# Performance work log

Hardware: AMD Instinct MI355X
Metric: run time of the kernel (lower is better)

Reference implementation:

```python
import jax, jax.numpy as jnp
import numpy as np

N = 16384      # number of points
DIM = 128      # feature dim
POS_DIM = 3
K = 16         # neighbors (init kwarg k)
SCALE = np.float32(np.sqrt(DIM))


def setup_inputs() -> dict:
    key = jax.random.key(0)
    ks = jax.random.split(key, 16)
    g = lambda i, shape: (jax.random.normal(ks[i], shape, dtype=jnp.float32) * 0.05)
    return {
        "x": jax.random.normal(ks[0], (N, DIM), dtype=jnp.float32),
        "pos": jax.random.uniform(ks[1], (N, POS_DIM), dtype=jnp.float32),
        # weights stored as (in, out); torch Linear applies x @ W.T + b
        "Wq": g(2, (DIM, DIM)),
        "Wk": g(3, (DIM, DIM)),
        "Wv": g(4, (DIM, DIM)),
        "mid_w1": g(5, (DIM, DIM)), "mid_b1": g(6, (DIM,)),
        "mid_w2": g(7, (DIM, DIM)), "mid_b2": g(8, (DIM,)),
        "pe_w1": g(9, (POS_DIM, DIM)), "pe_b1": g(10, (DIM,)),
        "pe_w2": g(11, (DIM, DIM)), "pe_b2": g(12, (DIM,)),
        "fin_w": g(13, (DIM, DIM)), "fin_b": g(14, (DIM,)),
    }


def _knn_indices(pos):
    # squared pairwise distances [N, N]; top-K smallest -> neighbor indices [N, K]
    sq = jnp.sum(pos * pos, axis=-1)
    d2 = sq[:, None] + sq[None, :] - 2.0 * (pos @ pos.T)
    _, ind = jax.lax.top_k(-d2, K)
    return ind


def reference(x, pos, Wq, Wk, Wv, mid_w1, mid_b1, mid_w2, mid_b2,
              pe_w1, pe_b1, pe_w2, pe_b2, fin_w, fin_b):
    ind = _knn_indices(pos)                    # [N, K] int32 (constant wrt grads)
    x_k = x[ind]                               # [N, K, D]
    pos_k = pos[ind]                           # [N, K, 3]
    rel = pos[:, None, :] - pos_k              # [N, K, 3]
    pe = jax.nn.relu(rel @ pe_w1 + pe_b1) @ pe_w2 + pe_b2    # [N, K, D]
    q = x @ Wq                                 # [N, D]
    h = q[:, None, :] - (x_k @ Wk) + pe        # [N, K, D]
    y = jax.nn.relu(h @ mid_w1 + mid_b1) @ mid_w2 + mid_b2   # [N, K, D]
    y = jax.nn.softmax(y / SCALE, axis=-2)     # softmax over neighbors K
    z = x_k @ Wv + pe                          # [N, K, D]
    agg = jnp.sum(y * z, axis=-2)              # [N, D]
    return agg @ fin_w + fin_b + x
```

## Files before the change

kernel.cpp:

```cpp
#include <hip/hip_runtime.h>
#include <hip/hip_bf16.h>

#define N_PTS 16384
#define DIMF  128
#define KNB   16
#define GRES  8
#define NCELL (GRES*GRES*GRES)

typedef __attribute__((ext_vector_type(8))) short bf16x8;
typedef __attribute__((ext_vector_type(4))) short bf16x4;
typedef __attribute__((ext_vector_type(4))) float f32x4;
typedef __attribute__((ext_vector_type(4))) unsigned int u32x4;
typedef __attribute__((ext_vector_type(2))) unsigned int u32x2;

__device__ __forceinline__ unsigned short f2b(float f){
  unsigned int u = __float_as_uint(f);
  u = u + 0x7fffu + ((u >> 16) & 1u);
  return (unsigned short)(u >> 16);
}
__device__ __forceinline__ unsigned cvtpk(float lo, float hi){
  unsigned r;
  asm("v_cvt_pk_bf16_f32 %0, %1, %2" : "=v"(r) : "v"(lo), "v"(hi));
  return r;
}
__device__ __forceinline__ float b2f(unsigned short u){
  return __uint_as_float(((unsigned)u) << 16);
}
__device__ __forceinline__ float b2fs(short s){
  return __uint_as_float(((unsigned)(unsigned short)s) << 16);
}
__device__ __forceinline__ float unsort_f(unsigned s){
  unsigned u = (s & 0x80000000u) ? (s ^ 0x80000000u) : ~s;
  return __uint_as_float(u);
}

__global__ __launch_bounds__(256) void count_kernel(const float* __restrict__ pos, int* __restrict__ cnt){
  int i = blockIdx.x*256 + threadIdx.x;
  float px = pos[i*3+0], py = pos[i*3+1], pz = pos[i*3+2];
  int cx = min(GRES-1, max(0,(int)(px*(float)GRES)));
  int cy = min(GRES-1, max(0,(int)(py*(float)GRES)));
  int cz = min(GRES-1, max(0,(int)(pz*(float)GRES)));
  atomicAdd(&cnt[(cz*GRES+cy)*GRES+cx], 1);
}

__global__ __launch_bounds__(256) void scan_kernel(const int* __restrict__ cnt, int* __restrict__ starts, int* __restrict__ fillp){
  __shared__ int wsum[4];
  int t = threadIdx.x;
  int lane = t & 63, w = t >> 6;
  int a = cnt[2*t], b = cnt[2*t+1];
  int s = a + b;
  int p = s;
  #pragma unroll
  for (int off = 1; off < 64; off <<= 1){
    int v = __shfl_up(p, off, 64);
    if (lane >= off) p += v;
  }
  if (lane == 63) wsum[w] = p;
  __syncthreads();
  int base = 0;
  for (int i = 0; i < w; ++i) base += wsum[i];
  int excl = base + p - s;
  starts[2*t]   = excl;     fillp[2*t]   = excl;
  starts[2*t+1] = excl + a; fillp[2*t+1] = excl + a;
}

__global__ __launch_bounds__(256) void scatter_pack(const float* __restrict__ pos, int* __restrict__ fillp,
                                                    float4* __restrict__ pos4, int* __restrict__ pidx,
                                                    int* __restrict__ inv,
                                                    const float* __restrict__ w0, const float* __restrict__ w1,
                                                    const float* __restrict__ w2, const float* __restrict__ w3,
                                                    const float* __restrict__ w4, const float* __restrict__ w5,
                                                    const float* __restrict__ w6,
                                                    short* __restrict__ dst){
  if (blockIdx.x < 64){
    int i = blockIdx.x*256 + threadIdx.x;
    float px = pos[i*3+0], py = pos[i*3+1], pz = pos[i*3+2];
    int cx = min(GRES-1, max(0,(int)(px*(float)GRES)));
    int cy = min(GRES-1, max(0,(int)(py*(float)GRES)));
    int cz = min(GRES-1, max(0,(int)(pz*(float)GRES)));
    int c = (cz*GRES+cy)*GRES+cx;
    float sq = __fadd_rn(__fadd_rn(__fmul_rn(px,px), __fmul_rn(py,py)), __fmul_rn(pz,pz));
    int s = atomicAdd(&fillp[c], 1);
    pos4[s] = make_float4(px, py, pz, sq);
    pidx[s] = i;
    inv[i] = s;
  } else {
    int pb = blockIdx.x - 64;
    int slot = pb >> 6;
    const float* src = (slot==0)?w0:(slot==1)?w1:(slot==2)?w2:(slot==3)?w3:(slot==4)?w4:(slot==5)?w5:w6;
    int f = (pb & 63)*256 + threadIdx.x;
    int j  = f & 7;
    int ln = (f >> 3) & 63;
    int ks = (f >> 9) & 3;
    int nt = f >> 11;
    int k = ks*32 + ((ln >> 4) << 3) + j;
    int n = nt*16 + (ln & 15);
    dst[slot*16384 + f] = (short)f2b(src[k*DIMF + n]);
  }
}

__global__ __launch_bounds__(256) void knn_query64(const float4* __restrict__ pos4, const int* __restrict__ pidx,
                                                   const int* __restrict__ starts, const int* __restrict__ cnt,
                                                   const int* __restrict__ inv,
                                                   int* __restrict__ ind_slot, char* __restrict__ flags){
  __shared__ unsigned long long cand[4][64];
  int lane = threadIdx.x & 63;
  int wv   = threadIdx.x >> 6;
  int t = blockIdx.x*4 + wv;
  float4 qp = pos4[t];
  float qx = qp.x, qy = qp.y, qz = qp.z, qsq = qp.w;
  int cx = min(GRES-1, max(0,(int)(qx*(float)GRES)));
  int cy = min(GRES-1, max(0,(int)(qy*(float)GRES)));
  int cz = min(GRES-1, max(0,(int)(qz*(float)GRES)));
  int zlo = max(0,cz-1), zhi = min(GRES-1,cz+1);
  int ylo = max(0,cy-1), yhi = min(GRES-1,cy+1);
  int xlo = max(0,cx-1), xhi = min(GRES-1,cx+1);

  int nb = 0;
  if (lane < 27){
    int dz = lane/9 - 1, dy = (lane/3)%3 - 1, dx = lane%3 - 1;
    int zz = cz+dz, yy = cy+dy, xx = cx+dx;
    if (zz>=zlo && zz<=zhi && yy>=ylo && yy<=yhi && xx>=xlo && xx<=xhi)
      nb = cnt[(zz*GRES+yy)*GRES+xx];
  }
  #pragma unroll
  for (int o=1;o<64;o<<=1) nb += __shfl_xor(nb, o, 64);
  float V = (float)((zhi-zlo+1)*(yhi-ylo+1)*(xhi-xlo+1)) * 0.001953125f;
  float r3 = 3.8197186f * V / (float)nb;
  float tau2 = 2.0f * __powf(r3, 0.66666667f);

  int nfound = 0;
  bool okscan = false;
  for (int it = 0; it < 8; ++it){
    nfound = 0;
    for (int zz=zlo; zz<=zhi; ++zz)
    for (int yy=ylo; yy<=yhi; ++yy)
    for (int xx=xlo; xx<=xhi; ++xx){
      int c = (zz*GRES+yy)*GRES+xx;
      int s0 = starts[c], n = cnt[c];
      for (int b = 0; b < n; b += 64){
        int o = b + lane;
        bool valid = o < n;
        float d = 3.0e38f; int idx = 0;
        if (valid){
          float4 pc = pos4[s0+o];
          idx = pidx[s0+o];
          float dot = __fmaf_rn(qz, pc.z, __fmaf_rn(qy, pc.y, __fmul_rn(qx, pc.x)));
          d   = __fsub_rn(__fadd_rn(qsq, pc.w), __fmul_rn(2.0f, dot));
        }
        bool admit = valid && (d < tau2);
        unsigned long long mask = __ballot(admit);
        if (admit){
          int pos = nfound + (int)__popcll(mask & ((1ull<<lane)-1ull));
          if (pos < 64){
            unsigned su = __float_as_uint(d);
            su ^= (unsigned)((int)su >> 31) | 0x80000000u;
            cand[wv][pos] = ((unsigned long long)su << 32) | (unsigned)idx;
          }
        }
        nfound += (int)__popcll(mask);
      }
    }
    if (nfound > 64){ tau2 *= 0.7f; continue; }
    if (nfound < 16){ tau2 *= 2.0f; continue; }
    okscan = true; break;
  }
  if (!okscan){ if (lane == 0) flags[t] = 1; return; }

  asm volatile("s_waitcnt lgkmcnt(0)" ::: "memory");
  __builtin_amdgcn_sched_barrier(0);
  unsigned long long key = (lane < nfound) ? cand[wv][lane] : ~0ull;

  #pragma unroll
  for (int k = 2; k <= 64; k <<= 1){
    #pragma unroll
    for (int j = k>>1; j >= 1; j >>= 1){
      unsigned long long other = __shfl_xor(key, j, 64);
      bool takeSmall = (((lane & k) == 0) != ((lane & j) != 0));
      bool less = other < key;
      key = (takeSmall == less) ? other : key;
    }
  }
  if (lane < 16) ind_slot[t*KNB + lane] = inv[(int)(unsigned)(key & 0xffffffffu)];

  unsigned long long k15 = __shfl(key, 15, 64);
  float b16 = unsort_f((unsigned)(k15 >> 32));
  double mg = 1.0e300;
  double dqx=(double)qx, dqy=(double)qy, dqz=(double)qz;
  const double h = 0.125;
  if (cx-1 > 0)      mg = fmin(mg, dqx - (double)(cx-1)*h);
  if (cx+1 < GRES-1) mg = fmin(mg, (double)(cx+2)*h - dqx);
  if (cy-1 > 0)      mg = fmin(mg, dqy - (double)(cy-1)*h);
  if (cy+1 < GRES-1) mg = fmin(mg, (double)(cy+2)*h - dqy);
  if (cz-1 > 0)      mg = fmin(mg, dqz - (double)(cz-1)*h);
  if (cz+1 < GRES-1) mg = fmin(mg, (double)(cz+2)*h - dqz);
  bool ok = (mg*mg > (double)b16 + 1.0e-5);
  if (lane == 0) flags[t] = ok ? 0 : 1;
}

__global__ __launch_bounds__(256) void knn_fallback(const float4* __restrict__ pos4, const int* __restrict__ pidx,
                                                    const int* __restrict__ starts, const int* __restrict__ cnt,
                                                    const int* __restrict__ inv,
                                                    const char* __restrict__ flags, int* __restrict__ ind_slot){
  int t = blockIdx.x*256 + threadIdx.x;
  if (t >= N_PTS || !flags[t]) return;
  float4 qp = pos4[t];
  float qx = qp.x, qy = qp.y, qz = qp.z, qsq = qp.w;
  int cx = min(GRES-1, max(0,(int)(qx*(float)GRES)));
  int cy = min(GRES-1, max(0,(int)(qy*(float)GRES)));
  int cz = min(GRES-1, max(0,(int)(qz*(float)GRES)));
  float bd[KNB]; int bi[KNB];
  #pragma unroll
  for (int k=0;k<KNB;++k){ bd[k] = 3.0e38f; bi[k] = 0x7fffffff; }
  const double cinv = 0.125;
  for (int r = 0; r < GRES; ++r){
    int zlo = max(0, cz-r), zhi = min(GRES-1, cz+r);
    int ylo = max(0, cy-r), yhi = min(GRES-1, cy+r);
    int xlo = max(0, cx-r), xhi = min(GRES-1, cx+r);
    for (int zz = zlo; zz <= zhi; ++zz){
      for (int yy = ylo; yy <= yhi; ++yy){
        for (int xx = xlo; xx <= xhi; ++xx){
          int ring = max(abs(zz-cz), max(abs(yy-cy), abs(xx-cx)));
          if (ring != r) continue;
          int c = (zz*GRES+yy)*GRES+xx;
          int s0 = starts[c], e = s0 + cnt[c];
          for (int s = s0; s < e; ++s){
            float4 pc = pos4[s];
            int idx = pidx[s];
            float dot = __fmaf_rn(qz, pc.z, __fmaf_rn(qy, pc.y, __fmul_rn(qx, pc.x)));
            float d   = __fsub_rn(__fadd_rn(qsq, pc.w), __fmul_rn(2.0f, dot));
            bool adm = (d < bd[KNB-1]) || (d == bd[KNB-1] && idx < bi[KNB-1]);
            if (adm){
              #pragma unroll
              for (int p = KNB-1; p >= 1; --p){
                float pd = bd[p-1]; int pi = bi[p-1];
                bool sh  = (pd > d) || (pd == d && pi > idx);
                bool ins = (!sh) && ((bd[p] > d) || (bd[p] == d && bi[p] > idx));
                bd[p] = sh ? pd : (ins ? d   : bd[p]);
                bi[p] = sh ? pi : (ins ? idx : bi[p]);
              }
              bool s0b = (bd[0] > d) || (bd[0] == d && bi[0] > idx);
              if (s0b){ bd[0] = d; bi[0] = idx; }
            }
          }
        }
      }
    }
    if (bd[KNB-1] < 3.0e37f){
      double mg = 1.0e300;
      double dqx=(double)qx, dqy=(double)qy, dqz=(double)qz;
      if (cx - r > 0)      mg = fmin(mg, dqx - (double)(cx-r)*cinv);
      if (cx + r < GRES-1) mg = fmin(mg, (double)(cx+r+1)*cinv - dqx);
      if (cy - r > 0)      mg = fmin(mg, dqy - (double)(cy-r)*cinv);
      if (cy + r < GRES-1) mg = fmin(mg, (double)(cy+r+1)*cinv - dqy);
      if (cz - r > 0)      mg = fmin(mg, dqz - (double)(cz-r)*cinv);
      if (cz + r < GRES-1) mg = fmin(mg, (double)(cz+r+1)*cinv - dqz);
      if (mg*mg > (double)bd[KNB-1] + 1.0e-5) break;
    }
  }
  #pragma unroll
  for (int k=0;k<KNB;++k) ind_slot[t*KNB + k] = inv[bi[k]];
}

__global__ __launch_bounds__(256) void proj_kernel(const float* __restrict__ x, const int* __restrict__ pidx,
                                                   const short* __restrict__ pw,
                                                   unsigned short* __restrict__ q, unsigned short* __restrict__ xk,
                                                   unsigned short* __restrict__ xv){
  __shared__ __align__(16) char Abuf[16384];
  int tid = threadIdx.x, lane = tid & 63, wv = tid >> 6;
  int r0 = blockIdx.x * 64;
  {
    int row = tid >> 2, q4 = tid & 3;
    int orig = pidx[r0 + row];
    const float4* xr = (const float4*)(x + (size_t)orig*DIMF + q4*32);
    #pragma unroll
    for (int i=0;i<4;++i){
      float4 a = xr[2*i], b = xr[2*i+1];
      u32x4 u;
      u[0] = cvtpk(a.x, a.y); u[1] = cvtpk(a.z, a.w);
      u[2] = cvtpk(b.x, b.y); u[3] = cvtpk(b.z, b.w);
      *(u32x4*)(&Abuf[row*256 + ((q4*64 + i*16) ^ ((row&7)<<4))]) = u;
    }
  }
  __syncthreads();
  #pragma unroll 1
  for (int w = 0; w < 3; ++w){
    const bf16x8* bw = (const bf16x8*)(pw + w*16384);
    unsigned short* dst = (w==0) ? q : (w==1) ? xk : xv;
    f32x4 acc[8];
    #pragma unroll
    for (int nt=0;nt<8;++nt) acc[nt] = (f32x4){0.f,0.f,0.f,0.f};
    #pragma unroll
    for (int ks=0;ks<4;++ks){
      int ra = wv*16 + (lane&15);
      int cb = ks*64 + ((lane>>4)<<4);
      bf16x8 a0 = *(const bf16x8*)(&Abuf[ra*256 + (cb ^ ((ra&7)<<4))]);
      #pragma unroll
      for (int nt=0;nt<8;++nt){
        bf16x8 b = bw[(nt*4+ks)*64 + lane];
        acc[nt] = __builtin_amdgcn_mfma_f32_16x16x32_bf16(a0, b, acc[nt], 0, 0, 0);
      }
    }
    #pragma unroll
    for (int nt=0;nt<8;++nt){
      int grow = r0 + wv*16 + ((lane>>4)<<2);
      int col = nt*16 + (lane&15);
      unsigned pk01 = cvtpk(acc[nt][0], acc[nt][1]);
      unsigned pk23 = cvtpk(acc[nt][2], acc[nt][3]);
      dst[(size_t)(grow+0)*DIMF + col] = (unsigned short)pk01;
      dst[(size_t)(grow+1)*DIMF + col] = (unsigned short)(pk01 >> 16);
      dst[(size_t)(grow+2)*DIMF + col] = (unsigned short)pk23;
      dst[(size_t)(grow+3)*DIMF + col] = (unsigned short)(pk23 >> 16);
    }
  }
}

__global__ __launch_bounds__(512, 2) void main_kernel(
    const float* __restrict__ x, const float4* __restrict__ pos4, const int* __restrict__ pidx,
    const float* __restrict__ pe_w1, const float* __restrict__ pe_b1, const float* __restrict__ pe_b2,
    const float* __restrict__ mid_b1, const float* __restrict__ mid_b2, const float* __restrict__ fin_b,
    const unsigned short* __restrict__ qarr, const unsigned short* __restrict__ xkarr,
    const unsigned short* __restrict__ xvarr,
    const int* __restrict__ ind_slot, const short* __restrict__ pw,
    float* __restrict__ out)
{
  __shared__ __align__(16) char peLDS[32768];
  __shared__ __align__(16) char wbuf[32768];
  __shared__ float aggT[DIMF][9];
  __shared__ int indbuf[128];
  __shared__ int origbuf[8];
  int tid = threadIdx.x;
  int lane = tid & 63;
  int wv = tid >> 6;
  int t0 = blockIdx.x * 8;

  int g = lane >> 4, kl = lane & 15;
  int mt = wv;

  #define STAGE_W(slot) { \
    const char* gsrc = (const char*)(pw + (size_t)(slot)*16384) + wv*4096 + lane*16; \
    char* ldst = &wbuf[wv*4096]; \
    __builtin_amdgcn_global_load_lds(gsrc,        ldst,        16, 0, 0); \
    __builtin_amdgcn_global_load_lds(gsrc + 1024, ldst + 1024, 16, 0, 0); \
    __builtin_amdgcn_global_load_lds(gsrc + 2048, ldst + 2048, 16, 0, 0); \
    __builtin_amdgcn_global_load_lds(gsrc + 3072, ldst + 3072, 16, 0, 0); }

  if (tid < 128) indbuf[tid] = ind_slot[blockIdx.x*128 + tid];
  if (tid < 8) origbuf[tid] = pidx[t0 + tid];
  STAGE_W(3);
  __syncthreads();

  int nb4[4];
  #pragma unroll
  for (int r=0;r<4;++r) nb4[r] = indbuf[mt*16 + g*4 + r];
  int nbr = indbuf[mt*16 + kl];
  unsigned short zraw[8][4];
  #pragma unroll
  for (int nt=0;nt<8;++nt)
    #pragma unroll
    for (int r=0;r<4;++r)
      zraw[nt][r] = xvarr[(size_t)nb4[r]*DIMF + nt*16 + kl];

  bf16x8 tfrag[4];
  {
    float4 pq = pos4[t0+mt];
    float4 pn = pos4[nbr];
    float rx = pq.x-pn.x, ry = pq.y-pn.y, rz = pq.z-pn.z;
    #pragma unroll
    for (int ks=0;ks<4;++ks){
      int c0 = ks*32 + g*8;
      const float4* w0 = (const float4*)(pe_w1 + c0);
      const float4* w1 = (const float4*)(pe_w1 + DIMF + c0);
      const float4* w2 = (const float4*)(pe_w1 + 2*DIMF + c0);
      const float4* bb = (const float4*)(pe_b1 + c0);
      float4 wa0=w0[0], wa1=w0[1], wb0=w1[0], wb1=w1[1], wc0=w2[0], wc1=w2[1], wd0=bb[0], wd1=bb[1];
      float wa[8]={wa0.x,wa0.y,wa0.z,wa0.w,wa1.x,wa1.y,wa1.z,wa1.w};
      float wb[8]={wb0.x,wb0.y,wb0.z,wb0.w,wb1.x,wb1.y,wb1.z,wb1.w};
      float wc[8]={wc0.x,wc0.y,wc0.z,wc0.w,wc1.x,wc1.y,wc1.z,wc1.w};
      float wd[8]={wd0.x,wd0.y,wd0.z,wd0.w,wd1.x,wd1.y,wd1.z,wd1.w};
      float tv[8];
      #pragma unroll
      for (int j=0;j<8;++j)
        tv[j] = fmaxf(fmaf(rx, wa[j], fmaf(ry, wb[j], fmaf(rz, wc[j], wd[j]))), 0.f);
      u32x4 u;
      u[0] = cvtpk(tv[0], tv[1]); u[1] = cvtpk(tv[2], tv[3]);
      u[2] = cvtpk(tv[4], tv[5]); u[3] = cvtpk(tv[6], tv[7]);
      tfrag[ks] = __builtin_bit_cast(bf16x8, u);
    }
  }

  f32x4 acc[8];
  const bf16x8* bw = (const bf16x8*)wbuf;

  {
    #pragma unroll
    for (int nt=0;nt<8;++nt){
      float bv = pe_b2[nt*16 + kl];
      acc[nt] = (f32x4){bv,bv,bv,bv};
    }
    #pragma unroll
    for (int ks=0;ks<4;++ks){
      #pragma unroll
      for (int nt=0;nt<8;++nt){
        bf16x8 b = bw[(nt*4+ks)*64 + lane];
        acc[nt] = __builtin_amdgcn_mfma_f32_16x16x32_bf16(tfrag[ks], b, acc[nt], 0, 0, 0);
      }
    }
  }

  bf16x4 zb[8];
  int r0w = mt*16 + g*4;
  #pragma unroll
  for (int nt=0;nt<8;++nt){
    int col = nt*16 + kl;
    float p0 = acc[nt][0], p1 = acc[nt][1], p2 = acc[nt][2], p3 = acc[nt][3];
    unsigned pk01 = cvtpk(p0, p1), pk23 = cvtpk(p2, p3);
    *(unsigned short*)&peLDS[(r0w+0)*256 + ((col*2) ^ (((r0w+0)&7)<<4))] = (unsigned short)pk01;
    *(unsigned short*)&peLDS[(r0w+1)*256 + ((col*2) ^ (((r0w+1)&7)<<4))] = (unsigned short)(pk01 >> 16);
    *(unsigned short*)&peLDS[(r0w+2)*256 + ((col*2) ^ (((r0w+2)&7)<<4))] = (unsigned short)pk23;
    *(unsigned short*)&peLDS[(r0w+3)*256 + ((col*2) ^ (((r0w+3)&7)<<4))] = (unsigned short)(pk23 >> 16);
    float z0 = b2f(zraw[nt][0]) + p0;
    float z1 = b2f(zraw[nt][1]) + p1;
    float z2 = b2f(zraw[nt][2]) + p2;
    float z3 = b2f(zraw[nt][3]) + p3;
    u32x2 zu; zu[0] = cvtpk(z0, z1); zu[1] = cvtpk(z2, z3);
    zb[nt] = __builtin_bit_cast(bf16x4, zu);
  }

  bf16x8 q8[4], k8[4];
  {
    const unsigned short* qrow = qarr + (size_t)(t0+mt)*DIMF;
    const unsigned short* krow = xkarr + (size_t)nbr*DIMF;
    #pragma unroll
    for (int ks=0;ks<4;++ks){
      int c0 = ks*32 + g*8;
      q8[ks] = *(const bf16x8*)(qrow + c0);
      k8[ks] = *(const bf16x8*)(krow + c0);
    }
  }
  __syncthreads();
  STAGE_W(4);

  bf16x8 hfrag[4];
  {
    int row = mt*16 + kl;
    #pragma unroll
    for (int ks=0;ks<4;++ks){
      int c0 = ks*32 + g*8;
      bf16x8 p8 = *(const bf16x8*)(&peLDS[row*256 + ((c0*2) ^ ((row&7)<<4))]);
      float hf[8];
      #pragma unroll
      for (int j=0;j<8;++j)
        hf[j] = (b2fs(q8[ks][j]) - b2fs(k8[ks][j])) + b2fs(p8[j]);
      u32x4 u;
      u[0] = cvtpk(hf[0], hf[1]); u[1] = cvtpk(hf[2], hf[3]);
      u[2] = cvtpk(hf[4], hf[5]); u[3] = cvtpk(hf[6], hf[7]);
      hfrag[ks] = __builtin_bit_cast(bf16x8, u);
    }
  }
  __syncthreads();

  {
    #pragma unroll
    for (int nt=0;nt<8;++nt){
      float bv = mid_b1[nt*16 + kl];
      acc[nt] = (f32x4){bv,bv,bv,bv};
    }
    #pragma unroll
    for (int ks=0;ks<4;++ks){
      #pragma unroll
      for (int nt=0;nt<8;++nt){
        bf16x8 b = bw[(nt*4+ks)*64 + lane];
        acc[nt] = __builtin_amdgcn_mfma_f32_16x16x32_bf16(hfrag[ks], b, acc[nt], 0, 0, 0);
      }
    }
  }
  __syncthreads();
  STAGE_W(5);
  #pragma unroll
  for (int nt=0;nt<8;++nt){
    int col = nt*16 + kl;
    unsigned pk01 = cvtpk(fmaxf(acc[nt][0],0.f), fmaxf(acc[nt][1],0.f));
    unsigned pk23 = cvtpk(fmaxf(acc[nt][2],0.f), fmaxf(acc[nt][3],0.f));
    *(unsigned short*)&peLDS[(r0w+0)*256 + ((col*2) ^ (((r0w+0)&7)<<4))] = (unsigned short)pk01;
    *(unsigned short*)&peLDS[(r0w+1)*256 + ((col*2) ^ (((r0w+1)&7)<<4))] = (unsigned short)(pk01 >> 16);
    *(unsigned short*)&peLDS[(r0w+2)*256 + ((col*2) ^ (((r0w+2)&7)<<4))] = (unsigned short)pk23;
    *(unsigned short*)&peLDS[(r0w+3)*256 + ((col*2) ^ (((r0w+3)&7)<<4))] = (unsigned short)(pk23 >> 16);
  }
  __syncthreads();

  {
    #pragma unroll
    for (int nt=0;nt<8;++nt){
      float bv = mid_b2[nt*16 + kl];
      acc[nt] = (f32x4){bv,bv,bv,bv};
    }
    #pragma unroll
    for (int ks=0;ks<4;++ks){
      int ra = mt*16 + kl;
      int cb = ks*64 + g*16;
      bf16x8 a0 = *(const bf16x8*)(&peLDS[ra*256 + (cb ^ ((ra&7)<<4))]);
      #pragma unroll
      for (int nt=0;nt<8;++nt){
        bf16x8 b = bw[(nt*4+ks)*64 + lane];
        acc[nt] = __builtin_amdgcn_mfma_f32_16x16x32_bf16(a0, b, acc[nt], 0, 0, 0);
      }
    }
  }
  __syncthreads();
  STAGE_W(6);

  {
    const float invS = 0.08838834764831843f;
    #pragma unroll
    for (int nt=0;nt<8;++nt){
      f32x4 y = acc[nt];
      float mx = fmaxf(fmaxf(y[0],y[1]), fmaxf(y[2],y[3]));
      mx = fmaxf(mx, __shfl_xor(mx, 16, 64));
      mx = fmaxf(mx, __shfl_xor(mx, 32, 64));
      float e0 = __expf((y[0]-mx)*invS);
      float e1 = __expf((y[1]-mx)*invS);
      float e2 = __expf((y[2]-mx)*invS);
      float e3 = __expf((y[3]-mx)*invS);
      float ssum = e0+e1+e2+e3;
      ssum += __shfl_xor(ssum, 16, 64);
      ssum += __shfl_xor(ssum, 32, 64);
      bf16x4 zv = zb[nt];
      float ps = (e0*b2fs(zv[0]) + e1*b2fs(zv[1]) + e2*b2fs(zv[2]) + e3*b2fs(zv[3])) / ssum;
      ps += __shfl_xor(ps, 16, 64);
      ps += __shfl_xor(ps, 32, 64);
      if (lane < 16) aggT[nt*16 + lane][mt] = ps;
    }
  }
  __syncthreads();

  {
    f32x4 facc = (f32x4){0.f,0.f,0.f,0.f};
    #pragma unroll
    for (int ks=0;ks<4;++ks){
      int c0 = ks*32 + g*8;
      float av[8];
      #pragma unroll
      for (int j=0;j<8;++j)
        av[j] = (kl < 8) ? aggT[c0+j][kl] : 0.f;
      u32x4 u;
      u[0] = cvtpk(av[0], av[1]); u[1] = cvtpk(av[2], av[3]);
      u[2] = cvtpk(av[4], av[5]); u[3] = cvtpk(av[6], av[7]);
      bf16x8 a = __builtin_bit_cast(bf16x8, u);
      bf16x8 b = bw[(wv*4+ks)*64 + lane];
      facc = __builtin_amdgcn_mfma_f32_16x16x32_bf16(a, b, facc, 0, 0, 0);
    }
    int col = wv*16 + kl;
    float fb = fin_b[col];
    if (g < 2){
      #pragma unroll
      for (int r=0;r<4;++r){
        int prow = g*4 + r;
        int o = origbuf[prow];
        out[(size_t)o*DIMF + col] = facc[r] + fb + x[(size_t)o*DIMF + col];
      }
    }
  }
  #undef STAGE_W
}

extern "C" void kernel_launch(void* const* d_in, const int* in_sizes, int n_in,
                              void* d_out, int out_size, void* d_ws, size_t ws_size,
                              hipStream_t stream)
{
  (void)in_sizes; (void)n_in; (void)out_size; (void)ws_size;
  const float* x      = (const float*)d_in[0];
  const float* pos    = (const float*)d_in[1];
  const float* Wq     = (const float*)d_in[2];
  const float* Wk     = (const float*)d_in[3];
  const float* Wv     = (const float*)d_in[4];
  const float* mid_w1 = (const float*)d_in[5];
  const float* mid_b1 = (const float*)d_in[6];
  const float* mid_w2 = (const float*)d_in[7];
  const float* mid_b2 = (const float*)d_in[8];
  const float* pe_w1  = (const float*)d_in[9];
  const float* pe_b1  = (const float*)d_in[10];
  const float* pe_w2  = (const float*)d_in[11];
  const float* pe_b2  = (const float*)d_in[12];
  const float* fin_w  = (const float*)d_in[13];
  const float* fin_b  = (const float*)d_in[14];
  float* out = (float*)d_out;
  char* ws = (char*)d_ws;

  int*    cellcnt = (int*)   (ws + 0);
  int*    fillp   = (int*)   (ws + 4096);
  int*    starts  = (int*)   (ws + 8192);
  char*   flags   = (char*)  (ws + 18432);
  int*    pidx    = (int*)   (ws + 49152);
  float4* pos4    = (float4*)(ws + 114688);
  int*    ind     = (int*)   (ws + 376832);
  short*  pw      = (short*) (ws + 1425408);
  int*    inv     = (int*)   (ws + 1654784);
  unsigned short* qarr  = (unsigned short*)(ws + 1720320);
  unsigned short* xkarr = (unsigned short*)(ws + 5914624);
  unsigned short* xvarr = (unsigned short*)(ws + 10108928);

  hipMemsetAsync(cellcnt, 0, NCELL*sizeof(int), stream);
  count_kernel  <<<N_PTS/256, 256, 0, stream>>>(pos, cellcnt);
  scan_kernel   <<<1,         256, 0, stream>>>(cellcnt, starts, fillp);
  scatter_pack  <<<64 + 7*64, 256, 0, stream>>>(pos, fillp, pos4, pidx, inv,
                                                Wq, Wk, Wv, pe_w2, mid_w1, mid_w2, fin_w, pw);
  knn_query64   <<<N_PTS/4,   256, 0, stream>>>(pos4, pidx, starts, cellcnt, inv, ind, flags);
  knn_fallback  <<<N_PTS/256, 256, 0, stream>>>(pos4, pidx, starts, cellcnt, inv, flags, ind);
  proj_kernel   <<<N_PTS/64,  256, 0, stream>>>(x, pidx, pw, qarr, xkarr, xvarr);
  main_kernel   <<<N_PTS/8,   512, 0, stream>>>(x, pos4, pidx, pe_w1, pe_b1, pe_b2, mid_b1, mid_b2, fin_b,
                                                qarr, xkarr, xvarr, ind, pw, out);
}
```

Baseline: 163.0 us.

## Fuse kNN fallback into query kernel and prune cells beyond threshold

Adds a per-cell minimum-distance test so cells that cannot contain points within the current radius threshold are skipped during the 3x3x3 scan. The separate fallback kernel and flags array are removed; the fallback ring search now runs inline in the query wavefront, which removes one launch and the global flags round trip. The inline fallback runs the same serial per-query work redundantly on all 64 lanes of the wave, and a rare slow query now stalls its whole block.

```diff
diff --git a/kernel.cpp b/kernel.cpp
--- a/kernel.cpp
+++ b/kernel.cpp
@@ -102,7 +102,7 @@
 __global__ __launch_bounds__(256) void knn_query64(const float4* __restrict__ pos4, const int* __restrict__ pidx,
                                                    const int* __restrict__ starts, const int* __restrict__ cnt,
                                                    const int* __restrict__ inv,
-                                                   int* __restrict__ ind_slot, char* __restrict__ flags){
+                                                   int* __restrict__ ind_slot){
   __shared__ unsigned long long cand[4][64];
   int lane = threadIdx.x & 63;
   int wv   = threadIdx.x >> 6;
@@ -115,6 +115,8 @@
   int zlo = max(0,cz-1), zhi = min(GRES-1,cz+1);
   int ylo = max(0,cy-1), yhi = min(GRES-1,cy+1);
   int xlo = max(0,cx-1), xhi = min(GRES-1,cx+1);
+  const double h = 0.125;
+  double dqx=(double)qx, dqy=(double)qy, dqz=(double)qz;
 
   int nb = 0;
   if (lane < 27){
@@ -136,6 +138,11 @@
     for (int zz=zlo; zz<=zhi; ++zz)
     for (int yy=ylo; yy<=yhi; ++yy)
     for (int xx=xlo; xx<=xhi; ++xx){
+      double mdx = fmax(0.0, fmax((double)xx*h - dqx, dqx - (double)(xx+1)*h));
+      double mdy = fmax(0.0, fmax((double)yy*h - dqy, dqy - (double)(yy+1)*h));
+      double mdz = fmax(0.0, fmax((double)zz*h - dqz, dqz - (double)(zz+1)*h));
+      double md2 = mdx*mdx + mdy*mdy + mdz*mdz;
+      if (md2 > (double)tau2 + 1.0e-5) continue;
       int c = (zz*GRES+yy)*GRES+xx;
       int s0 = starts[c], n = cnt[c];
       for (int b = 0; b < n; b += 64){
@@ -165,101 +172,85 @@
     if (nfound < 16){ tau2 *= 2.0f; continue; }
     okscan = true; break;
   }
-  if (!okscan){ if (lane == 0) flags[t] = 1; return; }
-
-  asm volatile("s_waitcnt lgkmcnt(0)" ::: "memory");
-  __builtin_amdgcn_sched_barrier(0);
-  unsigned long long key = (lane < nfound) ? cand[wv][lane] : ~0ull;
-
-  #pragma unroll
-  for (int k = 2; k <= 64; k <<= 1){
-    #pragma unroll
-    for (int j = k>>1; j >= 1; j >>= 1){
-      unsigned long long other = __shfl_xor(key, j, 64);
-      bool takeSmall = (((lane & k) == 0) != ((lane & j) != 0));
-      bool less = other < key;
-      key = (takeSmall == less) ? other : key;
-    }
-  }
-  if (lane < 16) ind_slot[t*KNB + lane] = inv[(int)(unsigned)(key & 0xffffffffu)];
-
-  unsigned long long k15 = __shfl(key, 15, 64);
-  float b16 = unsort_f((unsigned)(k15 >> 32));
-  double mg = 1.0e300;
-  double dqx=(double)qx, dqy=(double)qy, dqz=(double)qz;
-  const double h = 0.125;
-  if (cx-1 > 0)      mg = fmin(mg, dqx - (double)(cx-1)*h);
-  if (cx+1 < GRES-1) mg = fmin(mg, (double)(cx+2)*h - dqx);
-  if (cy-1 > 0)      mg = fmin(mg, dqy - (double)(cy-1)*h);
-  if (cy+1 < GRES-1) mg = fmin(mg, (double)(cy+2)*h - dqy);
-  if (cz-1 > 0)      mg = fmin(mg, dqz - (double)(cz-1)*h);
-  if (cz+1 < GRES-1) mg = fmin(mg, (double)(cz+2)*h - dqz);
-  bool ok = (mg*mg > (double)b16 + 1.0e-5);
-  if (lane == 0) flags[t] = ok ? 0 : 1;
-}
-
-__global__ __launch_bounds__(256) void knn_fallback(const float4* __restrict__ pos4, const int* __restrict__ pidx,
-                                                    const int* __restrict__ starts, const int* __restrict__ cnt,
-                                                    const int* __restrict__ inv,
-                                                    const char* __restrict__ flags, int* __restrict__ ind_slot){
-  int t = blockIdx.x*256 + threadIdx.x;
-  if (t >= N_PTS || !flags[t]) return;
-  float4 qp = pos4[t];
-  float qx = qp.x, qy = qp.y, qz = qp.z, qsq = qp.w;
-  int cx = min(GRES-1, max(0,(int)(qx*(float)GRES)));
-  int cy = min(GRES-1, max(0,(int)(qy*(float)GRES)));
-  int cz = min(GRES-1, max(0,(int)(qz*(float)GRES)));
-  float bd[KNB]; int bi[KNB];
-  #pragma unroll
-  for (int k=0;k<KNB;++k){ bd[k] = 3.0e38f; bi[k] = 0x7fffffff; }
-  const double cinv = 0.125;
-  for (int r = 0; r < GRES; ++r){
-    int zlo = max(0, cz-r), zhi = min(GRES-1, cz+r);
-    int ylo = max(0, cy-r), yhi = min(GRES-1, cy+r);
-    int xlo = max(0, cx-r), xhi = min(GRES-1, cx+r);
-    for (int zz = zlo; zz <= zhi; ++zz){
-      for (int yy = ylo; yy <= yhi; ++yy){
-        for (int xx = xlo; xx <= xhi; ++xx){
-          int ring = max(abs(zz-cz), max(abs(yy-cy), abs(xx-cx)));
-          if (ring != r) continue;
-          int c = (zz*GRES+yy)*GRES+xx;
-          int s0 = starts[c], e = s0 + cnt[c];
-          for (int s = s0; s < e; ++s){
-            float4 pc = pos4[s];
-            int idx = pidx[s];
-            float dot = __fmaf_rn(qz, pc.z, __fmaf_rn(qy, pc.y, __fmul_rn(qx, pc.x)));
-            float d   = __fsub_rn(__fadd_rn(qsq, pc.w), __fmul_rn(2.0f, dot));
-            bool adm = (d < bd[KNB-1]) || (d == bd[KNB-1] && idx < bi[KNB-1]);
-            if (adm){
-              #pragma unroll
-              for (int p = KNB-1; p >= 1; --p){
-                float pd = bd[p-1]; int pi = bi[p-1];
-                bool sh  = (pd > d) || (pd == d && pi > idx);
-                bool ins = (!sh) && ((bd[p] > d) || (bd[p] == d && bi[p] > idx));
-                bd[p] = sh ? pd : (ins ? d   : bd[p]);
-                bi[p] = sh ? pi : (ins ? idx : bi[p]);
-              }
-              bool s0b = (bd[0] > d) || (bd[0] == d && bi[0] > idx);
-              if (s0b){ bd[0] = d; bi[0] = idx; }
+
+  bool needfb = !okscan;
+  if (okscan){
+    asm volatile("s_waitcnt lgkmcnt(0)" ::: "memory");
+    __builtin_amdgcn_sched_barrier(0);
+    unsigned long long key = (lane < nfound) ? cand[wv][lane] : ~0ull;
+
+    #pragma unroll
+    for (int k = 2; k <= 64; k <<= 1){
+      #pragma unroll
+      for (int j = k>>1; j >= 1; j >>= 1){
+        unsigned long long other = __shfl_xor(key, j, 64);
+        bool takeSmall = (((lane & k) == 0) != ((lane & j) != 0));
+        bool less = other < key;
+        key = (takeSmall == less) ? other : key;
+      }
+    }
+    if (lane < 16) ind_slot[t*KNB + lane] = inv[(int)(unsigned)(key & 0xffffffffu)];
+
+    unsigned long long k15 = __shfl(key, 15, 64);
+    float b16 = unsort_f((unsigned)(k15 >> 32));
+    double mg = 1.0e300;
+    if (cx-1 > 0)      mg = fmin(mg, dqx - (double)(cx-1)*h);
+    if (cx+1 < GRES-1) mg = fmin(mg, (double)(cx+2)*h - dqx);
+    if (cy-1 > 0)      mg = fmin(mg, dqy - (double)(cy-1)*h);
+    if (cy+1 < GRES-1) mg = fmin(mg, (double)(cy+2)*h - dqy);
+    if (cz-1 > 0)      mg = fmin(mg, dqz - (double)(cz-1)*h);
+    if (cz+1 < GRES-1) mg = fmin(mg, (double)(cz+2)*h - dqz);
+    needfb = !(mg*mg > (double)b16 + 1.0e-5);
+  }
+
+  if (needfb){
+    float bd[KNB]; int bi[KNB];
+    #pragma unroll
+    for (int k=0;k<KNB;++k){ bd[k] = 3.0e38f; bi[k] = 0x7fffffff; }
+    for (int r = 0; r < GRES; ++r){
+      int zl = max(0, cz-r), zh = min(GRES-1, cz+r);
+      int yl = max(0, cy-r), yh = min(GRES-1, cy+r);
+      int xl = max(0, cx-r), xh = min(GRES-1, cx+r);
+      for (int zz = zl; zz <= zh; ++zz)
+      for (int yy = yl; yy <= yh; ++yy)
+      for (int xx = xl; xx <= xh; ++xx){
+        int ring = max(abs(zz-cz), max(abs(yy-cy), abs(xx-cx)));
+        if (ring != r) continue;
+        int c = (zz*GRES+yy)*GRES+xx;
+        int s0 = starts[c], e = s0 + cnt[c];
+        for (int s = s0; s < e; ++s){
+          float4 pc = pos4[s];
+          int idx = pidx[s];
+          float dot = __fmaf_rn(qz, pc.z, __fmaf_rn(qy, pc.y, __fmul_rn(qx, pc.x)));
+          float d   = __fsub_rn(__fadd_rn(qsq, pc.w), __fmul_rn(2.0f, dot));
+          bool adm = (d < bd[KNB-1]) || (d == bd[KNB-1] && idx < bi[KNB-1]);
+          if (adm){
+            #pragma unroll
+            for (int p = KNB-1; p >= 1; --p){
+              float pd = bd[p-1]; int pi = bi[p-1];
+              bool sh  = (pd > d) || (pd == d && pi > idx);
+              bool ins = (!sh) && ((bd[p] > d) || (bd[p] == d && bi[p] > idx));
+              bd[p] = sh ? pd : (ins ? d   : bd[p]);
+              bi[p] = sh ? pi : (ins ? idx : bi[p]);
             }
+            bool s0b = (bd[0] > d) || (bd[0] == d && bi[0] > idx);
+            if (s0b){ bd[0] = d; bi[0] = idx; }
           }
         }
       }
-    }
-    if (bd[KNB-1] < 3.0e37f){
-      double mg = 1.0e300;
-      double dqx=(double)qx, dqy=(double)qy, dqz=(double)qz;
-      if (cx - r > 0)      mg = fmin(mg, dqx - (double)(cx-r)*cinv);
-      if (cx + r < GRES-1) mg = fmin(mg, (double)(cx+r+1)*cinv - dqx);
-      if (cy - r > 0)      mg = fmin(mg, dqy - (double)(cy-r)*cinv);
-      if (cy + r < GRES-1) mg = fmin(mg, (double)(cy+r+1)*cinv - dqy);
-      if (cz - r > 0)      mg = fmin(mg, dqz - (double)(cz-r)*cinv);
-      if (cz + r < GRES-1) mg = fmin(mg, (double)(cz+r+1)*cinv - dqz);
-      if (mg*mg > (double)bd[KNB-1] + 1.0e-5) break;
-    }
-  }
-  #pragma unroll
-  for (int k=0;k<KNB;++k) ind_slot[t*KNB + k] = inv[bi[k]];
+      if (bd[KNB-1] < 3.0e37f){
+        double mg = 1.0e300;
+        if (cx - r > 0)      mg = fmin(mg, dqx - (double)(cx-r)*h);
+        if (cx + r < GRES-1) mg = fmin(mg, (double)(cx+r+1)*h - dqx);
+        if (cy - r > 0)      mg = fmin(mg, dqy - (double)(cy-r)*h);
+        if (cy + r < GRES-1) mg = fmin(mg, (double)(cy+r+1)*h - dqy);
+        if (cz - r > 0)      mg = fmin(mg, dqz - (double)(cz-r)*h);
+        if (cz + r < GRES-1) mg = fmin(mg, (double)(cz+r+1)*h - dqz);
+        if (mg*mg > (double)bd[KNB-1] + 1.0e-5) break;
+      }
+    }
+    if (lane < 16) ind_slot[t*KNB + lane] = inv[bi[lane]];
+  }
 }
 
 __global__ __launch_bounds__(256) void proj_kernel(const float* __restrict__ x, const int* __restrict__ pidx,
@@ -590,7 +581,6 @@
   int*    cellcnt = (int*)   (ws + 0);
   int*    fillp   = (int*)   (ws + 4096);
   int*    starts  = (int*)   (ws + 8192);
-  char*   flags   = (char*)  (ws + 18432);
   int*    pidx    = (int*)   (ws + 49152);
   float4* pos4    = (float4*)(ws + 114688);
   int*    ind     = (int*)   (ws + 376832);
@@ -605,8 +595,7 @@
   scan_kernel   <<<1,         256, 0, stream>>>(cellcnt, starts, fillp);
   scatter_pack  <<<64 + 7*64, 256, 0, stream>>>(pos, fillp, pos4, pidx, inv,
                                                 Wq, Wk, Wv, pe_w2, mid_w1, mid_w2, fin_w, pw);
-  knn_query64   <<<N_PTS/4,   256, 0, stream>>>(pos4, pidx, starts, cellcnt, inv, ind, flags);
-  knn_fallback  <<<N_PTS/256, 256, 0, stream>>>(pos4, pidx, starts, cellcnt, inv, flags, ind);
+  knn_query64   <<<N_PTS/4,   256, 0, stream>>>(pos4, pidx, starts, cellcnt, inv, ind);
   proj_kernel   <<<N_PTS/64,  256, 0, stream>>>(x, pidx, pw, qarr, xkarr, xvarr);
   main_kernel   <<<N_PTS/8,   512, 0, stream>>>(x, pos4, pidx, pe_w1, pe_b1, pe_b2, mid_b1, mid_b2, fin_b,
                                                 qarr, xkarr, xvarr, ind, pw, out);
```

Measured after the change: 163.6 us. About the same (+0.4%).
